# Kernel tuning notes

Measured on AMD Instinct MI355X. Metric: run time of the kernel, lower is better.

The kernel has to match this reference:

```python
import jax, jax.numpy as jnp
import numpy as np

B, LT, LS = 4, 1024, 1024
D, H, HKV, HD, FF = 2048, 32, 8, 64, 8192
BASE, EPS = 10000.0, 1e-6


def _rope(x):
    # x: [B, L, H, hd]; interleaved (even/odd) RoPE with positions = arange(L)
    L, d = x.shape[1], x.shape[-1]
    inv = 1.0 / (BASE ** (jnp.arange(0, d, 2, dtype=jnp.float32) / d))
    f = jnp.arange(L, dtype=jnp.float32)[:, None] * inv[None, :]  # [L, d/2]
    cos = jnp.cos(f)[None, :, None, :]
    sin = jnp.sin(f)[None, :, None, :]
    xe, xo = x[..., 0::2], x[..., 1::2]
    # stack -> [..., d/2, 2] -> reshape interleaves back to even/odd slots
    return jnp.stack([xe * cos - xo * sin, xe * sin + xo * cos], axis=-1).reshape(x.shape)


def _rmsnorm(x, g):
    return x * jax.lax.rsqrt(jnp.mean(x * x, axis=-1, keepdims=True) + EPS) * g


def _attn(q_in, k_in, v_in, Wq, Wk, Wv, Wo, bo, keep, use_rope):
    Bq, Lq, _ = q_in.shape
    Lk = k_in.shape[1]
    Q = (q_in @ Wq).reshape(Bq, Lq, H, HD)
    K = (k_in @ Wk).reshape(Bq, Lk, HKV, HD)
    V = (v_in @ Wv).reshape(Bq, Lk, HKV, HD)
    if use_rope:
        Q = _rope(Q)
        K = _rope(K)
    g = H // HKV  # GQA head expansion: each kv head repeated g times consecutively
    K = jnp.repeat(K, g, axis=2)
    V = jnp.repeat(V, g, axis=2)
    s = jnp.einsum('bqhd,bkhd->bhqk', Q, K) / jnp.sqrt(jnp.float32(HD))
    s = jnp.where(keep, s, jnp.finfo(s.dtype).min)
    p = jax.nn.softmax(s, axis=-1)
    ctx = jnp.einsum('bhqk,bkhd->bqhd', p, V).reshape(Bq, Lq, H * HD)
    return ctx @ Wo + bo


def setup_inputs() -> dict:
    key = jax.random.key(0)
    ks = jax.random.split(key, 16)
    s = 0.02

    def rn(k, shp):
        return jax.random.normal(k, shp, jnp.float32) * s

    return dict(
        x=jax.random.normal(ks[0], (B, LT, D), jnp.float32),
        encoder_output=jax.random.normal(ks[1], (B, LS, D), jnp.float32),
        pad_mask=jnp.ones((B, 1, LT), bool),
        target_mask=jnp.tril(jnp.ones((LT, LT), bool)),
        cross_attn_pad_mask=jnp.ones((B, 1, LS), bool),
        Wq1=rn(ks[2], (D, D)), Wk1=rn(ks[3], (D, HKV * HD)), Wv1=rn(ks[4], (D, HKV * HD)),
        Wo1=rn(ks[5], (D, D)), bo1=jnp.zeros((D,), jnp.float32),
        Wq2=rn(ks[6], (D, D)), Wk2=rn(ks[7], (D, HKV * HD)), Wv2=rn(ks[8], (D, HKV * HD)),
        Wo2=rn(ks[9], (D, D)), bo2=jnp.zeros((D,), jnp.float32),
        g1=jnp.ones((D,), jnp.float32), g2=jnp.ones((D,), jnp.float32), g3=jnp.ones((D,), jnp.float32),
        w1=rn(ks[10], (D, FF)), b1=jnp.zeros((FF,), jnp.float32),
        w2=rn(ks[11], (D, FF)), b2=jnp.zeros((FF,), jnp.float32),
        w3=rn(ks[12], (FF, D)), b3=jnp.zeros((D,), jnp.float32),
    )


def reference(x, encoder_output, pad_mask, target_mask, cross_attn_pad_mask,
              Wq1, Wk1, Wv1, Wo1, bo1, Wq2, Wk2, Wv2, Wo2, bo2,
              g1, g2, g3, w1, b1, w2, b2, w3, b3):
    # merged keep masks per _merge_masks: causal [1,1,Lq,Lk] AND pad [B,1,1,Lk]
    keep_self = target_mask[None, None, :, :] & pad_mask[:, None, :, :]
    keep_cross = cross_attn_pad_mask[:, None, :, :]
    n = _rmsnorm(x, g1)
    x = x + _attn(n, n, n, Wq1, Wk1, Wv1, Wo1, bo1, keep_self, True)
    n = _rmsnorm(x, g2)
    x = x + _attn(n, encoder_output, encoder_output, Wq2, Wk2, Wv2, Wo2, bo2, keep_cross, False)
    n = _rmsnorm(x, g3)
    x = x + (jax.nn.silu(n @ w1 + b1) * (n @ w2 + b2)) @ w3 + b3
    return x
```

## Files before the change

kernel.cpp:

```cpp
#include <hip/hip_runtime.h>
#include <stdint.h>

#define BB 4
#define LSEQ 1024
#define DMODEL 2048
#define NH 32
#define NKV 8
#define HD 64
#define FFDIM 8192

typedef unsigned short ushort_t;
typedef __attribute__((ext_vector_type(8))) short bf16x8;
typedef __attribute__((ext_vector_type(4))) float f32x4;
typedef __attribute__((ext_vector_type(16))) float f32x16;
typedef __attribute__((ext_vector_type(8))) unsigned short ushort8;

__device__ __forceinline__ ushort_t f2bf(float f) {
  union { float f; unsigned u; } x; x.f = f;
  unsigned u = x.u;
  u += 0x7fffu + ((u >> 16) & 1u);
  return (ushort_t)(u >> 16);
}
__device__ __forceinline__ float bf2f(ushort_t h) {
  union { unsigned u; float f; } x; x.u = ((unsigned)h) << 16;
  return x.f;
}

typedef __attribute__((address_space(3))) unsigned char lds_u8_t;
typedef __attribute__((address_space(1))) const unsigned char glob_u8_t;
__device__ __forceinline__ void gload_lds16(const void* g, void* lds) {
  __builtin_amdgcn_global_load_lds((glob_u8_t*)g, (lds_u8_t*)lds, 16, 0, 0);
}

__global__ void conv_bf16_kernel(const float* __restrict__ in,
                                 ushort_t* __restrict__ out, int nchunks) {
  int i = blockIdx.x * 256 + threadIdx.x;
  if (i >= nchunks) return;
  float4 a = ((const float4*)in)[i * 2 + 0];
  float4 b = ((const float4*)in)[i * 2 + 1];
  ushort8 o;
  o[0]=f2bf(a.x); o[1]=f2bf(a.y); o[2]=f2bf(a.z); o[3]=f2bf(a.w);
  o[4]=f2bf(b.x); o[5]=f2bf(b.y); o[6]=f2bf(b.z); o[7]=f2bf(b.w);
  ((ushort8*)out)[i] = o;
}

__global__ void convT_kernel(const float* __restrict__ W, ushort_t* __restrict__ Wt,
                             int K, int N) {
  __shared__ float tile[64][65];
  const int k0 = blockIdx.y * 64, n0 = blockIdx.x * 64;
  const int t = threadIdx.x;
  const int r = t >> 2, c0 = (t & 3) * 16;
#pragma unroll
  for (int j = 0; j < 4; ++j) {
    float4 v = *(const float4*)&W[(size_t)(k0 + r) * N + n0 + c0 + j * 4];
    tile[r][c0 + j*4 + 0] = v.x; tile[r][c0 + j*4 + 1] = v.y;
    tile[r][c0 + j*4 + 2] = v.z; tile[r][c0 + j*4 + 3] = v.w;
  }
  __syncthreads();
#pragma unroll
  for (int it = 0; it < 2; ++it) {
    int ci = t + it * 256;
    int n = ci >> 3, kc = (ci & 7) * 8;
    ushort8 o;
#pragma unroll
    for (int j = 0; j < 8; ++j) o[j] = f2bf(tile[kc + j][n]);
    *(ushort8*)&Wt[(size_t)(n0 + n) * K + k0 + kc] = o;
  }
}

__global__ void rmsnorm_kernel(const float* __restrict__ x, const float* __restrict__ g,
                               ushort_t* __restrict__ out) {
  const int row = blockIdx.x, t = threadIdx.x;
  const float* xr = x + (size_t)row * DMODEL;
  float4 a = ((const float4*)xr)[t * 2 + 0];
  float4 b = ((const float4*)xr)[t * 2 + 1];
  float ssq = a.x*a.x + a.y*a.y + a.z*a.z + a.w*a.w
            + b.x*b.x + b.y*b.y + b.z*b.z + b.w*b.w;
#pragma unroll
  for (int d = 1; d < 64; d <<= 1) ssq += __shfl_xor(ssq, d);
  __shared__ float wsum[4];
  if ((t & 63) == 0) wsum[t >> 6] = ssq;
  __syncthreads();
  float tot = wsum[0] + wsum[1] + wsum[2] + wsum[3];
  float scale = rsqrtf(tot * (1.f / DMODEL) + 1e-6f);
  float4 ga = ((const float4*)g)[t * 2 + 0];
  float4 gb = ((const float4*)g)[t * 2 + 1];
  ushort8 o;
  o[0]=f2bf(a.x*scale*ga.x); o[1]=f2bf(a.y*scale*ga.y);
  o[2]=f2bf(a.z*scale*ga.z); o[3]=f2bf(a.w*scale*ga.w);
  o[4]=f2bf(b.x*scale*gb.x); o[5]=f2bf(b.y*scale*gb.y);
  o[6]=f2bf(b.z*scale*gb.z); o[7]=f2bf(b.w*scale*gb.w);
  ((ushort8*)(out + (size_t)row * DMODEL))[t] = o;
}

__global__ void rope_fill_kernel(float2* __restrict__ tab) {
  int i = blockIdx.x * 256 + threadIdx.x;
  if (i >= LSEQ * 32) return;
  int d2 = i & 31, l = i >> 5;
  float inv = expf(-((2.f * d2) / 64.f) * logf(10000.f));
  float f = (float)l * inv;
  tab[i] = make_float2(cosf(f), sinf(f));
}

__global__ void rope_apply_kernel(ushort_t* __restrict__ X, const float2* __restrict__ tab,
                                  int L, int nh, int nchunks) {
  int i = blockIdx.x * 256 + threadIdx.x;
  if (i >= nchunks) return;
  int c = i & 7;
  int tmp = i >> 3;
  int h = tmp % nh; tmp /= nh;
  int l = tmp % L;  tmp /= L;
  int b = tmp;
  ushort_t* p = X + (((size_t)(b * L + l) * nh + h) * HD) + c * 8;
  ushort8 v = *(ushort8*)p;
#pragma unroll
  for (int j = 0; j < 4; ++j) {
    int d2 = c * 4 + j;
    float2 cs = tab[l * 32 + d2];
    float e = bf2f(v[2*j]), o = bf2f(v[2*j+1]);
    v[2*j]   = f2bf(e * cs.x - o * cs.y);
    v[2*j+1] = f2bf(e * cs.y + o * cs.x);
  }
  *(ushort8*)p = v;
}

__global__ __launch_bounds__(256, 2) void gemm_bt(
    const ushort_t* __restrict__ A, const ushort_t* __restrict__ Bt,
    int M, int N, int K, int mode,
    const float* __restrict__ bias, const float* __restrict__ res,
    const ushort_t* __restrict__ aux, void* __restrict__ outp, int LkVT)
{
  __shared__ __align__(16) ushort_t As[128 * 64];
  __shared__ __align__(16) ushort_t Bs[128 * 64];
  const int tid = threadIdx.x;
  const int lane = tid & 63;
  const int wv = tid >> 6;
  const int wm = wv >> 1, wn = wv & 1;

  const int gx = gridDim.x, gy = gridDim.y;
  const int orig = blockIdx.y * gx + blockIdx.x;
  int m0, n0;
  if ((gx & 7) == 0) {
    const int xcd = orig & 7;
    const int loc = orig >> 3;
    const int cpx = gx >> 3;
    const int nl = loc / gy;
    const int ml = loc - nl * gy;
    n0 = (xcd * cpx + nl) * 128;
    m0 = ml * 128;
  } else {
    const int nwg = gx * gy;
    int swz = ((nwg & 7) == 0) ? ((orig & 7) * (nwg >> 3) + (orig >> 3)) : orig;
    m0 = (swz / gx) * 128;
    n0 = (swz % gx) * 128;
  }

  const int l31 = lane & 31, l5 = lane >> 5;
  const int ar = lane >> 3;
  const int ac = ((lane & 7) ^ ar) * 8;

  f32x16 acc[2][2];
#pragma unroll
  for (int i = 0; i < 2; ++i)
#pragma unroll
    for (int c = 0; c < 2; ++c)
#pragma unroll
      for (int r = 0; r < 16; ++r) acc[i][c][r] = 0.f;

  for (int k0 = 0; k0 < K; k0 += 64) {
#pragma unroll
    for (int it = 0; it < 4; ++it) {
      int cb = wv * 4 + it;
      int row = cb * 8 + ar;
      gload_lds16(A  + (size_t)(m0 + row) * K + k0 + ac, (void*)(As + cb * 512));
      gload_lds16(Bt + (size_t)(n0 + row) * K + k0 + ac, (void*)(Bs + cb * 512));
    }
    __syncthreads();
#pragma unroll
    for (int ks = 0; ks < 4; ++ks) {
      bf16x8 af[2], bfr[2];
#pragma unroll
      for (int mi = 0; mi < 2; ++mi) {
        const int row = wm * 64 + mi * 32 + l31;
        const int slot = ((ks * 2 + l5) ^ (row & 7));
        af[mi] = *(const bf16x8*)&As[row * 64 + slot * 8];
      }
#pragma unroll
      for (int ni = 0; ni < 2; ++ni) {
        const int row = wn * 64 + ni * 32 + l31;
        const int slot = ((ks * 2 + l5) ^ (row & 7));
        bfr[ni] = *(const bf16x8*)&Bs[row * 64 + slot * 8];
      }
#pragma unroll
      for (int mi = 0; mi < 2; ++mi)
#pragma unroll
        for (int ni = 0; ni < 2; ++ni)
          acc[mi][ni] = __builtin_amdgcn_mfma_f32_32x32x16_bf16(
              af[mi], bfr[ni], acc[mi][ni], 0, 0, 0);
    }
    __syncthreads();
  }

#pragma unroll
  for (int mi = 0; mi < 2; ++mi) {
#pragma unroll
    for (int ni = 0; ni < 2; ++ni) {
      const int col = n0 + wn * 64 + ni * 32 + l31;
      const float bv = bias ? bias[col] : 0.f;
      const int rb = m0 + wm * 64 + mi * 32 + 4 * l5;
      if (mode == 0) {
        ushort_t* ob = (ushort_t*)outp;
#pragma unroll
        for (int r = 0; r < 16; ++r)
          ob[(size_t)(rb + (r & 3) + 8 * (r >> 2)) * N + col] = f2bf(acc[mi][ni][r] + bv);
      } else if (mode == 1) {
        ushort_t* ob = (ushort_t*)outp;
#pragma unroll
        for (int r = 0; r < 16; ++r) {
          float t = acc[mi][ni][r] + bv;
          ob[(size_t)(rb + (r & 3) + 8 * (r >> 2)) * N + col] = f2bf(t / (1.f + __expf(-t)));
        }
      } else if (mode == 2) {
        ushort_t* ob = (ushort_t*)outp;
#pragma unroll
        for (int r = 0; r < 16; ++r) {
          size_t idx = (size_t)(rb + (r & 3) + 8 * (r >> 2)) * N + col;
          ob[idx] = f2bf((acc[mi][ni][r] + bv) * bf2f(aux[idx]));
        }
      } else if (mode == 3) {
        float* of = (float*)outp;
#pragma unroll
        for (int r = 0; r < 16; ++r) {
          size_t idx = (size_t)(rb + (r & 3) + 8 * (r >> 2)) * N + col;
          of[idx] = acc[mi][ni][r] + bv + res[idx];
        }
      } else {
        ushort_t* ob = (ushort_t*)outp;
        const int kvh = col >> 6, hd = col & 63;
#pragma unroll
        for (int r = 0; r < 16; ++r) {
          int row = rb + (r & 3) + 8 * (r >> 2);
          int b = row / LkVT, l = row - b * LkVT;
          ob[((size_t)((b * NKV + kvh) * HD + hd)) * LkVT + l] = f2bf(acc[mi][ni][r]);
        }
      }
    }
  }
}

__global__ __launch_bounds__(256, 2) void gemm_ffn12(
    const ushort_t* __restrict__ A, const ushort_t* __restrict__ B1t,
    const ushort_t* __restrict__ B2t, int M, int N, int K,
    const float* __restrict__ b1, const float* __restrict__ b2,
    ushort_t* __restrict__ outp)
{
  __shared__ __align__(16) ushort_t As[128 * 64];
  __shared__ __align__(16) ushort_t B1s[128 * 64];
  __shared__ __align__(16) ushort_t B2s[128 * 64];
  const int tid = threadIdx.x;
  const int lane = tid & 63;
  const int wv = tid >> 6;
  const int wm = wv >> 1, wn = wv & 1;

  const int gx = gridDim.x, gy = gridDim.y;
  const int orig = blockIdx.y * gx + blockIdx.x;
  const int xcd = orig & 7;
  const int loc = orig >> 3;
  const int cpx = gx >> 3;
  const int nl = loc / gy;
  const int ml = loc - nl * gy;
  const int n0 = (xcd * cpx + nl) * 128;
  const int m0 = ml * 128;

  const int l31 = lane & 31, l5 = lane >> 5;
  const int ar = lane >> 3;
  const int ac = ((lane & 7) ^ ar) * 8;

  f32x16 ac1[2][2], ac2[2][2];
#pragma unroll
  for (int i = 0; i < 2; ++i)
#pragma unroll
    for (int c = 0; c < 2; ++c)
#pragma unroll
      for (int r = 0; r < 16; ++r) { ac1[i][c][r] = 0.f; ac2[i][c][r] = 0.f; }

  for (int k0 = 0; k0 < K; k0 += 64) {
#pragma unroll
    for (int it = 0; it < 4; ++it) {
      int cb = wv * 4 + it;
      int row = cb * 8 + ar;
      gload_lds16(A   + (size_t)(m0 + row) * K + k0 + ac, (void*)(As  + cb * 512));
      gload_lds16(B1t + (size_t)(n0 + row) * K + k0 + ac, (void*)(B1s + cb * 512));
      gload_lds16(B2t + (size_t)(n0 + row) * K + k0 + ac, (void*)(B2s + cb * 512));
    }
    __syncthreads();
#pragma unroll
    for (int ks = 0; ks < 4; ++ks) {
      bf16x8 af[2], b1f[2], b2f[2];
#pragma unroll
      for (int mi = 0; mi < 2; ++mi) {
        const int row = wm * 64 + mi * 32 + l31;
        const int slot = ((ks * 2 + l5) ^ (row & 7));
        af[mi] = *(const bf16x8*)&As[row * 64 + slot * 8];
      }
#pragma unroll
      for (int ni = 0; ni < 2; ++ni) {
        const int row = wn * 64 + ni * 32 + l31;
        const int slot = ((ks * 2 + l5) ^ (row & 7));
        b1f[ni] = *(const bf16x8*)&B1s[row * 64 + slot * 8];
        b2f[ni] = *(const bf16x8*)&B2s[row * 64 + slot * 8];
      }
#pragma unroll
      for (int mi = 0; mi < 2; ++mi)
#pragma unroll
        for (int ni = 0; ni < 2; ++ni) {
          ac1[mi][ni] = __builtin_amdgcn_mfma_f32_32x32x16_bf16(
              af[mi], b1f[ni], ac1[mi][ni], 0, 0, 0);
          ac2[mi][ni] = __builtin_amdgcn_mfma_f32_32x32x16_bf16(
              af[mi], b2f[ni], ac2[mi][ni], 0, 0, 0);
        }
    }
    __syncthreads();
  }

#pragma unroll
  for (int mi = 0; mi < 2; ++mi) {
#pragma unroll
    for (int ni = 0; ni < 2; ++ni) {
      const int col = n0 + wn * 64 + ni * 32 + l31;
      const float bv1 = b1[col], bv2 = b2[col];
      const int rb = m0 + wm * 64 + mi * 32 + 4 * l5;
#pragma unroll
      for (int r = 0; r < 16; ++r) {
        float v1 = ac1[mi][ni][r] + bv1;
        float v2 = ac2[mi][ni][r] + bv2;
        float h = (v1 / (1.f + __expf(-v1))) * v2;
        outp[(size_t)(rb + (r & 3) + 8 * (r >> 2)) * N + col] = f2bf(h);
      }
    }
  }
}

template <bool CAUSAL>
__global__ __launch_bounds__(256) void attn_kernel(
    const ushort_t* __restrict__ Q, const ushort_t* __restrict__ Kb,
    const ushort_t* __restrict__ VT, ushort_t* __restrict__ ctx,
    int Lq, int Lk)
{
  __shared__ __align__(16) ushort_t Ks[64 * 72];
  __shared__ __align__(16) ushort_t Vs[64 * 72];
  __shared__ __align__(16) ushort_t Ps[4][16 * 72];

  const int tid = threadIdx.x;
  const int lane = tid & 63;
  const int w = tid >> 6;
  const int nqt = Lq >> 6;
  int bid = blockIdx.x;
  const int qt = bid % nqt; bid /= nqt;
  const int h = bid % NH;
  const int b = bid / NH;
  const int kv = h >> 2;
  const int q0 = qt * 64;
  const int l15 = lane & 15, l4 = lane >> 4;

  const ushort_t* qbase = Q + ((size_t)(b * Lq + q0 + w * 16 + l15) * NH + h) * HD;
  bf16x8 qf[2];
  qf[0] = *(const bf16x8*)(qbase + l4 * 8);
  qf[1] = *(const bf16x8*)(qbase + 32 + l4 * 8);

  f32x4 o[4];
#pragma unroll
  for (int d = 0; d < 4; ++d) o[d] = f32x4{0.f, 0.f, 0.f, 0.f};
  float mrow[4] = {-1e30f, -1e30f, -1e30f, -1e30f};
  float lrow[4] = {0.f, 0.f, 0.f, 0.f};

  const int nkt = CAUSAL ? (qt + 1) : (Lk >> 6);
  for (int kt = 0; kt < nkt; ++kt) {
#pragma unroll
    for (int it = 0; it < 2; ++it) {
      int ci = tid + it * 256;
      int r = ci >> 3, ch = (ci & 7) * 8;
      uint4 dk = *(const uint4*)(Kb + ((size_t)(b * Lk + kt * 64 + r) * NKV + kv) * HD + ch);
      *(uint4*)&Ks[r * 72 + ch] = dk;
      uint4 dv = *(const uint4*)(VT + ((size_t)((b * NKV + kv) * HD + r)) * Lk + kt * 64 + ch);
      *(uint4*)&Vs[r * 72 + ch] = dv;
    }
    __syncthreads();

    f32x4 s[4];
#pragma unroll
    for (int cb = 0; cb < 4; ++cb) {
      f32x4 a = f32x4{0.f, 0.f, 0.f, 0.f};
      a = __builtin_amdgcn_mfma_f32_16x16x32_bf16(
            qf[0], *(const bf16x8*)&Ks[(cb * 16 + l15) * 72 + l4 * 8], a, 0, 0, 0);
      a = __builtin_amdgcn_mfma_f32_16x16x32_bf16(
            qf[1], *(const bf16x8*)&Ks[(cb * 16 + l15) * 72 + 32 + l4 * 8], a, 0, 0, 0);
      s[cb] = a;
    }
    const bool diag = CAUSAL && (kt == qt);
#pragma unroll
    for (int cb = 0; cb < 4; ++cb) {
#pragma unroll
      for (int v = 0; v < 4; ++v) {
        float sv = s[cb][v] * 0.125f;
        if (diag) {
          int kpos = kt * 64 + cb * 16 + l15;
          int qpos = q0 + w * 16 + l4 * 4 + v;
          if (kpos > qpos) sv = -1e30f;
        }
        s[cb][v] = sv;
      }
    }
    float alpha[4];
#pragma unroll
    for (int v = 0; v < 4; ++v) {
      float m2 = fmaxf(fmaxf(s[0][v], s[1][v]), fmaxf(s[2][v], s[3][v]));
#pragma unroll
      for (int d = 1; d < 16; d <<= 1) m2 = fmaxf(m2, __shfl_xor(m2, d));
      float mn = fmaxf(mrow[v], m2);
      alpha[v] = __expf(mrow[v] - mn);
      mrow[v] = mn;
    }
    float psum[4] = {0.f, 0.f, 0.f, 0.f};
#pragma unroll
    for (int cb = 0; cb < 4; ++cb) {
#pragma unroll
      for (int v = 0; v < 4; ++v) {
        float p = __expf(s[cb][v] - mrow[v]);
        psum[v] += p;
        Ps[w][(l4 * 4 + v) * 72 + cb * 16 + l15] = f2bf(p);
      }
    }
#pragma unroll
    for (int v = 0; v < 4; ++v) lrow[v] = lrow[v] * alpha[v] + psum[v];
#pragma unroll
    for (int d = 0; d < 4; ++d)
#pragma unroll
      for (int v = 0; v < 4; ++v) o[d][v] *= alpha[v];

#pragma unroll
    for (int ks = 0; ks < 2; ++ks) {
      bf16x8 pa = *(const bf16x8*)&Ps[w][l15 * 72 + ks * 32 + l4 * 8];
#pragma unroll
      for (int d = 0; d < 4; ++d) {
        bf16x8 vf = *(const bf16x8*)&Vs[(d * 16 + l15) * 72 + ks * 32 + l4 * 8];
        o[d] = __builtin_amdgcn_mfma_f32_16x16x32_bf16(pa, vf, o[d], 0, 0, 0);
      }
    }
    __syncthreads();
  }

  float inv[4];
#pragma unroll
  for (int v = 0; v < 4; ++v) {
    float L = lrow[v];
#pragma unroll
    for (int d = 1; d < 16; d <<= 1) L += __shfl_xor(L, d);
    inv[v] = 1.f / L;
  }
  ushort_t* cbase = ctx + ((size_t)(b * Lq + q0 + w * 16) * NH + h) * HD;
#pragma unroll
  for (int d = 0; d < 4; ++d)
#pragma unroll
    for (int v = 0; v < 4; ++v) {
      int qloc = l4 * 4 + v;
      cbase[(size_t)qloc * NH * HD + d * 16 + l15] = f2bf(o[d][v] * inv[v]);
    }
}

extern "C" void kernel_launch(void* const* d_in, const int* in_sizes, int n_in,
                              void* d_out, int out_size, void* d_ws, size_t ws_size,
                              hipStream_t stream) {
  const float* x    = (const float*)d_in[0];
  const float* enc  = (const float*)d_in[1];
  const float* Wq1 = (const float*)d_in[5];
  const float* Wk1 = (const float*)d_in[6];
  const float* Wv1 = (const float*)d_in[7];
  const float* Wo1 = (const float*)d_in[8];
  const float* bo1 = (const float*)d_in[9];
  const float* Wq2 = (const float*)d_in[10];
  const float* Wk2 = (const float*)d_in[11];
  const float* Wv2 = (const float*)d_in[12];
  const float* Wo2 = (const float*)d_in[13];
  const float* bo2 = (const float*)d_in[14];
  const float* g1  = (const float*)d_in[15];
  const float* g2  = (const float*)d_in[16];
  const float* g3  = (const float*)d_in[17];
  const float* w1  = (const float*)d_in[18];
  const float* b1  = (const float*)d_in[19];
  const float* w2  = (const float*)d_in[20];
  const float* b2  = (const float*)d_in[21];
  const float* w3  = (const float*)d_in[22];
  const float* b3  = (const float*)d_in[23];

  const int M = BB * LSEQ;
  uint8_t* ws = (uint8_t*)d_ws;
  size_t off = 0;
  auto alloc = [&](size_t bytes) { void* p = ws + off; off += (bytes + 255) & ~(size_t)255; return p; };
  ushort_t* n_bf   = (ushort_t*)alloc((size_t)M * DMODEL * 2);
  ushort_t* enc_bf = (ushort_t*)alloc((size_t)M * DMODEL * 2);
  ushort_t* q_bf   = (ushort_t*)alloc((size_t)M * DMODEL * 2);
  ushort_t* k_bf   = (ushort_t*)alloc((size_t)M * NKV * HD * 2);
  ushort_t* vt_bf  = (ushort_t*)alloc((size_t)M * NKV * HD * 2);
  ushort_t* ctx_bf = (ushort_t*)alloc((size_t)M * DMODEL * 2);
  ushort_t* h_bf   = (ushort_t*)alloc((size_t)M * FFDIM * 2);
  ushort_t* wt     = (ushort_t*)alloc((size_t)DMODEL * FFDIM * 2);
  float2*   tab    = (float2*)alloc((size_t)LSEQ * 32 * 8);
  ushort_t* wt2    = enc_bf;
  (void)ws_size; (void)in_sizes; (void)n_in; (void)out_size;

  float* xf = (float*)d_out;

  conv_bf16_kernel<<<4096, 256, 0, stream>>>(enc, enc_bf, M * DMODEL / 8);
  rope_fill_kernel<<<128, 256, 0, stream>>>(tab);

  const int KVN = NKV * HD;
  dim3 blk(256);
  auto ggrid = [](int N, int Mm) { return dim3(N / 128, Mm / 128); };
  auto tgrid = [](int K, int N) { return dim3(N / 64, K / 64); };

  rmsnorm_kernel<<<M, 256, 0, stream>>>(x, g1, n_bf);
  convT_kernel<<<tgrid(DMODEL, DMODEL), blk, 0, stream>>>(Wq1, wt, DMODEL, DMODEL);
  gemm_bt<<<ggrid(DMODEL, M), blk, 0, stream>>>(n_bf, wt, M, DMODEL, DMODEL, 0, nullptr, nullptr, nullptr, q_bf, 1);
  convT_kernel<<<tgrid(DMODEL, KVN), blk, 0, stream>>>(Wk1, wt, DMODEL, KVN);
  gemm_bt<<<ggrid(KVN, M), blk, 0, stream>>>(n_bf, wt, M, KVN, DMODEL, 0, nullptr, nullptr, nullptr, k_bf, 1);
  rope_apply_kernel<<<(M * NH * 8) / 256, 256, 0, stream>>>(q_bf, tab, LSEQ, NH, M * NH * 8);
  rope_apply_kernel<<<(M * NKV * 8) / 256, 256, 0, stream>>>(k_bf, tab, LSEQ, NKV, M * NKV * 8);
  convT_kernel<<<tgrid(DMODEL, KVN), blk, 0, stream>>>(Wv1, wt, DMODEL, KVN);
  gemm_bt<<<ggrid(KVN, M), blk, 0, stream>>>(n_bf, wt, M, KVN, DMODEL, 4, nullptr, nullptr, nullptr, vt_bf, LSEQ);
  attn_kernel<true><<<BB * NH * (LSEQ / 64), blk, 0, stream>>>(q_bf, k_bf, vt_bf, ctx_bf, LSEQ, LSEQ);
  convT_kernel<<<tgrid(DMODEL, DMODEL), blk, 0, stream>>>(Wo1, wt, DMODEL, DMODEL);
  gemm_bt<<<ggrid(DMODEL, M), blk, 0, stream>>>(ctx_bf, wt, M, DMODEL, DMODEL, 3, bo1, x, nullptr, xf, 1);

  rmsnorm_kernel<<<M, 256, 0, stream>>>(xf, g2, n_bf);
  convT_kernel<<<tgrid(DMODEL, DMODEL), blk, 0, stream>>>(Wq2, wt, DMODEL, DMODEL);
  gemm_bt<<<ggrid(DMODEL, M), blk, 0, stream>>>(n_bf, wt, M, DMODEL, DMODEL, 0, nullptr, nullptr, nullptr, q_bf, 1);
  convT_kernel<<<tgrid(DMODEL, KVN), blk, 0, stream>>>(Wk2, wt, DMODEL, KVN);
  gemm_bt<<<ggrid(KVN, M), blk, 0, stream>>>(enc_bf, wt, M, KVN, DMODEL, 0, nullptr, nullptr, nullptr, k_bf, 1);
  convT_kernel<<<tgrid(DMODEL, KVN), blk, 0, stream>>>(Wv2, wt, DMODEL, KVN);
  gemm_bt<<<ggrid(KVN, M), blk, 0, stream>>>(enc_bf, wt, M, KVN, DMODEL, 4, nullptr, nullptr, nullptr, vt_bf, LSEQ);
  attn_kernel<false><<<BB * NH * (LSEQ / 64), blk, 0, stream>>>(q_bf, k_bf, vt_bf, ctx_bf, LSEQ, LSEQ);
  convT_kernel<<<tgrid(DMODEL, DMODEL), blk, 0, stream>>>(Wo2, wt, DMODEL, DMODEL);
  gemm_bt<<<ggrid(DMODEL, M), blk, 0, stream>>>(ctx_bf, wt, M, DMODEL, DMODEL, 3, bo2, xf, nullptr, xf, 1);

  rmsnorm_kernel<<<M, 256, 0, stream>>>(xf, g3, n_bf);
  convT_kernel<<<tgrid(DMODEL, FFDIM), blk, 0, stream>>>(w1, wt, DMODEL, FFDIM);
  convT_kernel<<<tgrid(DMODEL, FFDIM), blk, 0, stream>>>(w2, wt2, DMODEL, FFDIM);
  gemm_ffn12<<<ggrid(FFDIM, M), blk, 0, stream>>>(n_bf, wt, wt2, M, FFDIM, DMODEL, b1, b2, h_bf);
  convT_kernel<<<tgrid(FFDIM, DMODEL), blk, 0, stream>>>(w3, wt, FFDIM, DMODEL);
  gemm_bt<<<ggrid(DMODEL, M), blk, 0, stream>>>(h_bf, wt, M, DMODEL, FFDIM, 3, b3, xf, nullptr, xf, 1);
}
```

Before: 1.145 ms.

## Fuse Q/K/V projections into one GEMM and enlarge GEMM M-tile to 256

Concatenates the transposed Wq/Wk/Wv weights so the self-attention QKV projection runs as one GEMM with a split epilogue (mode 5), and the cross-attention K/V projection as one GEMM (mode 6). This removes separate launches and rereads of the normalized activations. It also doubles the gemm_bt tile height to 256 rows, with more accumulators per wave, for more reuse of each B tile. The cost is more LDS and register pressure, which may lower occupancy, and fewer workgroups for the smaller GEMMs. The unused silu and multiply epilogue modes are dropped.

After: 2.662 ms. 133% more time.

```diff
diff --git a/kernel.cpp b/kernel.cpp
--- a/kernel.cpp
+++ b/kernel.cpp
@@ -128,9 +128,10 @@
     const ushort_t* __restrict__ A, const ushort_t* __restrict__ Bt,
     int M, int N, int K, int mode,
     const float* __restrict__ bias, const float* __restrict__ res,
-    const ushort_t* __restrict__ aux, void* __restrict__ outp, int LkVT)
+    void* __restrict__ outp, void* __restrict__ out2, void* __restrict__ out3,
+    int LkVT)
 {
-  __shared__ __align__(16) ushort_t As[128 * 64];
+  __shared__ __align__(16) ushort_t As[256 * 64];
   __shared__ __align__(16) ushort_t Bs[128 * 64];
   const int tid = threadIdx.x;
   const int lane = tid & 63;
@@ -147,11 +148,11 @@
     const int nl = loc / gy;
     const int ml = loc - nl * gy;
     n0 = (xcd * cpx + nl) * 128;
-    m0 = ml * 128;
+    m0 = ml * 256;
   } else {
     const int nwg = gx * gy;
     int swz = ((nwg & 7) == 0) ? ((orig & 7) * (nwg >> 3) + (orig >> 3)) : orig;
-    m0 = (swz / gx) * 128;
+    m0 = (swz / gx) * 256;
     n0 = (swz % gx) * 128;
   }
 
@@ -159,29 +160,34 @@
   const int ar = lane >> 3;
   const int ac = ((lane & 7) ^ ar) * 8;
 
-  f32x16 acc[2][2];
-#pragma unroll
-  for (int i = 0; i < 2; ++i)
+  f32x16 acc[4][2];
+#pragma unroll
+  for (int i = 0; i < 4; ++i)
 #pragma unroll
     for (int c = 0; c < 2; ++c)
 #pragma unroll
       for (int r = 0; r < 16; ++r) acc[i][c][r] = 0.f;
 
   for (int k0 = 0; k0 < K; k0 += 64) {
+#pragma unroll
+    for (int it = 0; it < 8; ++it) {
+      int cb = wv * 8 + it;
+      int row = cb * 8 + ar;
+      gload_lds16(A + (size_t)(m0 + row) * K + k0 + ac, (void*)(As + cb * 512));
+    }
 #pragma unroll
     for (int it = 0; it < 4; ++it) {
       int cb = wv * 4 + it;
       int row = cb * 8 + ar;
-      gload_lds16(A  + (size_t)(m0 + row) * K + k0 + ac, (void*)(As + cb * 512));
       gload_lds16(Bt + (size_t)(n0 + row) * K + k0 + ac, (void*)(Bs + cb * 512));
     }
     __syncthreads();
 #pragma unroll
     for (int ks = 0; ks < 4; ++ks) {
-      bf16x8 af[2], bfr[2];
-#pragma unroll
-      for (int mi = 0; mi < 2; ++mi) {
-        const int row = wm * 64 + mi * 32 + l31;
+      bf16x8 af[4], bfr[2];
+#pragma unroll
+      for (int mi = 0; mi < 4; ++mi) {
+        const int row = wm * 128 + mi * 32 + l31;
         const int slot = ((ks * 2 + l5) ^ (row & 7));
         af[mi] = *(const bf16x8*)&As[row * 64 + slot * 8];
       }
@@ -192,7 +198,7 @@
         bfr[ni] = *(const bf16x8*)&Bs[row * 64 + slot * 8];
       }
 #pragma unroll
-      for (int mi = 0; mi < 2; ++mi)
+      for (int mi = 0; mi < 4; ++mi)
 #pragma unroll
         for (int ni = 0; ni < 2; ++ni)
           acc[mi][ni] = __builtin_amdgcn_mfma_f32_32x32x16_bf16(
@@ -202,46 +208,61 @@
   }
 
 #pragma unroll
-  for (int mi = 0; mi < 2; ++mi) {
+  for (int mi = 0; mi < 4; ++mi) {
 #pragma unroll
     for (int ni = 0; ni < 2; ++ni) {
       const int col = n0 + wn * 64 + ni * 32 + l31;
-      const float bv = bias ? bias[col] : 0.f;
-      const int rb = m0 + wm * 64 + mi * 32 + 4 * l5;
+      const int rb = m0 + wm * 128 + mi * 32 + 4 * l5;
       if (mode == 0) {
         ushort_t* ob = (ushort_t*)outp;
+        const float bv = bias ? bias[col] : 0.f;
 #pragma unroll
         for (int r = 0; r < 16; ++r)
           ob[(size_t)(rb + (r & 3) + 8 * (r >> 2)) * N + col] = f2bf(acc[mi][ni][r] + bv);
-      } else if (mode == 1) {
-        ushort_t* ob = (ushort_t*)outp;
-#pragma unroll
-        for (int r = 0; r < 16; ++r) {
-          float t = acc[mi][ni][r] + bv;
-          ob[(size_t)(rb + (r & 3) + 8 * (r >> 2)) * N + col] = f2bf(t / (1.f + __expf(-t)));
-        }
-      } else if (mode == 2) {
-        ushort_t* ob = (ushort_t*)outp;
-#pragma unroll
-        for (int r = 0; r < 16; ++r) {
-          size_t idx = (size_t)(rb + (r & 3) + 8 * (r >> 2)) * N + col;
-          ob[idx] = f2bf((acc[mi][ni][r] + bv) * bf2f(aux[idx]));
-        }
       } else if (mode == 3) {
         float* of = (float*)outp;
+        const float bv = bias[col];
 #pragma unroll
         for (int r = 0; r < 16; ++r) {
           size_t idx = (size_t)(rb + (r & 3) + 8 * (r >> 2)) * N + col;
           of[idx] = acc[mi][ni][r] + bv + res[idx];
         }
+      } else if (mode == 5) {
+        if (col < 2048) {
+          ushort_t* qo = (ushort_t*)outp;
+#pragma unroll
+          for (int r = 0; r < 16; ++r)
+            qo[(size_t)(rb + (r & 3) + 8 * (r >> 2)) * 2048 + col] = f2bf(acc[mi][ni][r]);
+        } else if (col < 2560) {
+          ushort_t* ko = (ushort_t*)out2;
+#pragma unroll
+          for (int r = 0; r < 16; ++r)
+            ko[(size_t)(rb + (r & 3) + 8 * (r >> 2)) * 512 + (col - 2048)] = f2bf(acc[mi][ni][r]);
+        } else {
+          ushort_t* vo = (ushort_t*)out3;
+          const int c2 = col - 2560, kvh = c2 >> 6, hd = c2 & 63;
+#pragma unroll
+          for (int r = 0; r < 16; ++r) {
+            int row = rb + (r & 3) + 8 * (r >> 2);
+            int b = row / LkVT, l = row - b * LkVT;
+            vo[((size_t)((b * NKV + kvh) * HD + hd)) * LkVT + l] = f2bf(acc[mi][ni][r]);
+          }
+        }
       } else {
-        ushort_t* ob = (ushort_t*)outp;
-        const int kvh = col >> 6, hd = col & 63;
-#pragma unroll
-        for (int r = 0; r < 16; ++r) {
-          int row = rb + (r & 3) + 8 * (r >> 2);
-          int b = row / LkVT, l = row - b * LkVT;
-          ob[((size_t)((b * NKV + kvh) * HD + hd)) * LkVT + l] = f2bf(acc[mi][ni][r]);
+        if (col < 512) {
+          ushort_t* ko = (ushort_t*)out2;
+#pragma unroll
+          for (int r = 0; r < 16; ++r)
+            ko[(size_t)(rb + (r & 3) + 8 * (r >> 2)) * 512 + col] = f2bf(acc[mi][ni][r]);
+        } else {
+          ushort_t* vo = (ushort_t*)out3;
+          const int c2 = col - 512, kvh = c2 >> 6, hd = c2 & 63;
+#pragma unroll
+          for (int r = 0; r < 16; ++r) {
+            int row = rb + (r & 3) + 8 * (r >> 2);
+            int b = row / LkVT, l = row - b * LkVT;
+            vo[((size_t)((b * NKV + kvh) * HD + hd)) * LkVT + l] = f2bf(acc[mi][ni][r]);
+          }
         }
       }
     }
@@ -516,37 +537,35 @@
 
   const int KVN = NKV * HD;
   dim3 blk(256);
-  auto ggrid = [](int N, int Mm) { return dim3(N / 128, Mm / 128); };
-  auto tgrid = [](int K, int N) { return dim3(N / 64, K / 64); };
+  auto ggrid  = [](int N, int Mm) { return dim3(N / 128, Mm / 256); };
+  auto ggridF = [](int N, int Mm) { return dim3(N / 128, Mm / 128); };
+  auto tgrid  = [](int K, int N) { return dim3(N / 64, K / 64); };
 
   rmsnorm_kernel<<<M, 256, 0, stream>>>(x, g1, n_bf);
   convT_kernel<<<tgrid(DMODEL, DMODEL), blk, 0, stream>>>(Wq1, wt, DMODEL, DMODEL);
-  gemm_bt<<<ggrid(DMODEL, M), blk, 0, stream>>>(n_bf, wt, M, DMODEL, DMODEL, 0, nullptr, nullptr, nullptr, q_bf, 1);
-  convT_kernel<<<tgrid(DMODEL, KVN), blk, 0, stream>>>(Wk1, wt, DMODEL, KVN);
-  gemm_bt<<<ggrid(KVN, M), blk, 0, stream>>>(n_bf, wt, M, KVN, DMODEL, 0, nullptr, nullptr, nullptr, k_bf, 1);
+  convT_kernel<<<tgrid(DMODEL, KVN), blk, 0, stream>>>(Wk1, wt + (size_t)2048 * DMODEL, DMODEL, KVN);
+  convT_kernel<<<tgrid(DMODEL, KVN), blk, 0, stream>>>(Wv1, wt + (size_t)2560 * DMODEL, DMODEL, KVN);
+  gemm_bt<<<ggrid(3072, M), blk, 0, stream>>>(n_bf, wt, M, 3072, DMODEL, 5, nullptr, nullptr, q_bf, k_bf, vt_bf, LSEQ);
   rope_apply_kernel<<<(M * NH * 8) / 256, 256, 0, stream>>>(q_bf, tab, LSEQ, NH, M * NH * 8);
   rope_apply_kernel<<<(M * NKV * 8) / 256, 256, 0, stream>>>(k_bf, tab, LSEQ, NKV, M * NKV * 8);
-  convT_kernel<<<tgrid(DMODEL, KVN), blk, 0, stream>>>(Wv1, wt, DMODEL, KVN);
-  gemm_bt<<<ggrid(KVN, M), blk, 0, stream>>>(n_bf, wt, M, KVN, DMODEL, 4, nullptr, nullptr, nullptr, vt_bf, LSEQ);
   attn_kernel<true><<<BB * NH * (LSEQ / 64), blk, 0, stream>>>(q_bf, k_bf, vt_bf, ctx_bf, LSEQ, LSEQ);
   convT_kernel<<<tgrid(DMODEL, DMODEL), blk, 0, stream>>>(Wo1, wt, DMODEL, DMODEL);
-  gemm_bt<<<ggrid(DMODEL, M), blk, 0, stream>>>(ctx_bf, wt, M, DMODEL, DMODEL, 3, bo1, x, nullptr, xf, 1);
+  gemm_bt<<<ggrid(DMODEL, M), blk, 0, stream>>>(ctx_bf, wt, M, DMODEL, DMODEL, 3, bo1, x, xf, nullptr, nullptr, 1);
 
   rmsnorm_kernel<<<M, 256, 0, stream>>>(xf, g2, n_bf);
   convT_kernel<<<tgrid(DMODEL, DMODEL), blk, 0, stream>>>(Wq2, wt, DMODEL, DMODEL);
-  gemm_bt<<<ggrid(DMODEL, M), blk, 0, stream>>>(n_bf, wt, M, DMODEL, DMODEL, 0, nullptr, nullptr, nullptr, q_bf, 1);
+  gemm_bt<<<ggrid(DMODEL, M), blk, 0, stream>>>(n_bf, wt, M, DMODEL, DMODEL, 0, nullptr, nullptr, q_bf, nullptr, nullptr, 1);
   convT_kernel<<<tgrid(DMODEL, KVN), blk, 0, stream>>>(Wk2, wt, DMODEL, KVN);
-  gemm_bt<<<ggrid(KVN, M), blk, 0, stream>>>(enc_bf, wt, M, KVN, DMODEL, 0, nullptr, nullptr, nullptr, k_bf, 1);
-  convT_kernel<<<tgrid(DMODEL, KVN), blk, 0, stream>>>(Wv2, wt, DMODEL, KVN);
-  gemm_bt<<<ggrid(KVN, M), blk, 0, stream>>>(enc_bf, wt, M, KVN, DMODEL, 4, nullptr, nullptr, nullptr, vt_bf, LSEQ);
+  convT_kernel<<<tgrid(DMODEL, KVN), blk, 0, stream>>>(Wv2, wt + (size_t)512 * DMODEL, DMODEL, KVN);
+  gemm_bt<<<ggrid(1024, M), blk, 0, stream>>>(enc_bf, wt, M, 1024, DMODEL, 6, nullptr, nullptr, nullptr, k_bf, vt_bf, LSEQ);
   attn_kernel<false><<<BB * NH * (LSEQ / 64), blk, 0, stream>>>(q_bf, k_bf, vt_bf, ctx_bf, LSEQ, LSEQ);
   convT_kernel<<<tgrid(DMODEL, DMODEL), blk, 0, stream>>>(Wo2, wt, DMODEL, DMODEL);
-  gemm_bt<<<ggrid(DMODEL, M), blk, 0, stream>>>(ctx_bf, wt, M, DMODEL, DMODEL, 3, bo2, xf, nullptr, xf, 1);
+  gemm_bt<<<ggrid(DMODEL, M), blk, 0, stream>>>(ctx_bf, wt, M, DMODEL, DMODEL, 3, bo2, xf, xf, nullptr, nullptr, 1);
 
   rmsnorm_kernel<<<M, 256, 0, stream>>>(xf, g3, n_bf);
   convT_kernel<<<tgrid(DMODEL, FFDIM), blk, 0, stream>>>(w1, wt, DMODEL, FFDIM);
   convT_kernel<<<tgrid(DMODEL, FFDIM), blk, 0, stream>>>(w2, wt2, DMODEL, FFDIM);
-  gemm_ffn12<<<ggrid(FFDIM, M), blk, 0, stream>>>(n_bf, wt, wt2, M, FFDIM, DMODEL, b1, b2, h_bf);
+  gemm_ffn12<<<ggridF(FFDIM, M), blk, 0, stream>>>(n_bf, wt, wt2, M, FFDIM, DMODEL, b1, b2, h_bf);
   convT_kernel<<<tgrid(FFDIM, DMODEL), blk, 0, stream>>>(w3, wt, FFDIM, DMODEL);
-  gemm_bt<<<ggrid(DMODEL, M), blk, 0, stream>>>(h_bf, wt, M, DMODEL, FFDIM, 3, b3, xf, nullptr, xf, 1);
-}
+  gemm_bt<<<ggrid(DMODEL, M), blk, 0, stream>>>(h_bf, wt, M, DMODEL, FFDIM, 3, b3, xf, xf, nullptr, nullptr, 1);
+}
```
